# Performance work log

Hardware: AMD Instinct MI355X
Metric: run time of the kernel (lower is better)

Reference implementation:

```python
import jax, jax.numpy as jnp
import numpy as np

B, L, D = 1, 2048, 1024
H = 16
HD = D // H
BETA = 0.08
EPS = 1e-6


def setup_inputs() -> dict:
    key = jax.random.key(0)
    ks = jax.random.split(key, 12)
    sc = 1.0 / np.sqrt(D)
    inp = {
        'x': jax.random.normal(ks[0], (B, L, D), dtype=jnp.float32),
        'Wq': jax.random.normal(ks[1], (D, D), dtype=jnp.float32) * sc,
        'bq': jnp.zeros((D,), jnp.float32),
        'Wk': jax.random.normal(ks[2], (D, D), dtype=jnp.float32) * sc,
        'bk': jnp.zeros((D,), jnp.float32),
        'Wv': jax.random.normal(ks[3], (D, D), dtype=jnp.float32) * sc,
        'bv': jnp.zeros((D,), jnp.float32),
        'Wo': jax.random.normal(ks[4], (D, D), dtype=jnp.float32) * sc,
        'bo': jnp.zeros((D,), jnp.float32),
        'Wp': jax.random.normal(ks[5], (2 * H, D), dtype=jnp.float32) * sc,
        'bp': jnp.zeros((2 * H,), jnp.float32),
        'gamma': jnp.full((H,), -2.197224577, jnp.float32),
    }
    return inp


def _split(t):  # [B,L,D] -> [B,H,L,hd]
    return t.reshape(B, L, H, HD).transpose(0, 2, 1, 3)


def reference(x, Wq, bq, Wk, bk, Wv, bv, Wo, bo, Wp, bp, gamma):
    q = _split(x @ Wq.T + bq)
    k = _split(x @ Wk.T + bk)
    v = _split(x @ Wv.T + bv)

    # phase features: [B,L,2H] -> [B,H,L,2], L2-normalized (torch F.normalize: x / max(||x||, eps))
    ph = (x @ Wp.T + bp).reshape(B, L, H, 2).transpose(0, 2, 1, 3)
    nrm = jnp.maximum(jnp.linalg.norm(ph, axis=-1, keepdims=True), EPS)
    ph = ph / nrm
    c, s = ph[..., 0], ph[..., 1]  # [B,H,L]

    # rank-2 Gram interference bias: cos(dphi) = c_i c_j + s_i s_j -> [B,H,L,L]
    inter = c[..., :, None] * c[..., None, :] + s[..., :, None] * s[..., None, :]
    head_gate = jax.nn.sigmoid(gamma) * BETA  # active_heads_mask all ones (fraction=1.0)
    bias = inter * head_gate[None, :, None, None]

    scores = jnp.einsum('bhqd,bhkd->bhqk', q, k) / jnp.sqrt(jnp.float32(HD)) + bias
    attn = jax.nn.softmax(scores, axis=-1)
    out = jnp.einsum('bhqk,bhkd->bhqd', attn, v)
    out = out.transpose(0, 2, 1, 3).reshape(B, L, D)
    return out @ Wo.T + bo
```

## Files before the change

### kernel.cpp

```cpp
#include <hip/hip_runtime.h>
#include <stdint.h>

typedef unsigned short u16;
typedef unsigned int u32;

#define L_SEQ 2048
#define DMODEL 1024
#define NHEAD 16

using f32x4 = __attribute__((ext_vector_type(4))) float;
using f32x16 = __attribute__((ext_vector_type(16))) float;
using s16x8 = __attribute__((ext_vector_type(8))) short;
using s16x4 = __attribute__((ext_vector_type(4))) short;

__device__ __forceinline__ u16 f2b(float f) {
    union { float f; uint32_t u; } v; v.f = f;
    uint32_t r = v.u + 0x7fffu + ((v.u >> 16) & 1u);
    return (u16)(r >> 16);
}

__device__ __forceinline__ float b2f(u16 x) {
    union { uint32_t u; float f; } v; v.u = ((uint32_t)x) << 16;
    return v.f;
}

__device__ __forceinline__ u32 pk2(float a, float b) {
    return (u32)f2b(a) | ((u32)f2b(b) << 16);
}

__device__ __forceinline__ u32 cvtpk(float lo, float hi_) {
    u32 r;
    asm("v_cvt_pk_bf16_f32 %0, %1, %2" : "=v"(r) : "v"(lo), "v"(hi_));
    return r;
}

__device__ __forceinline__ void gld16(const void* g, void* l) {
    __builtin_amdgcn_global_load_lds(
        (__attribute__((address_space(1))) void*)(uintptr_t)g,
        (__attribute__((address_space(3))) void*)(uintptr_t)l,
        16, 0, 0);
}

__global__ __launch_bounds__(256)
void k_pre(const float* __restrict__ x, const float* __restrict__ wq,
           const float* __restrict__ wk, const float* __restrict__ wv,
           const float* __restrict__ wo,
           u16* __restrict__ xb, u16* __restrict__ wqb, u16* __restrict__ wkb,
           u16* __restrict__ wvb, u16* __restrict__ wob,
           const float* __restrict__ Wp, const float* __restrict__ bp,
           float2* __restrict__ CSph) {
    const int NX = L_SEQ * DMODEL / 8;
    const int NW = DMODEL * DMODEL / 8;
    const int NCONV = (NX + 4 * NW) / 256;
    const int tid = threadIdx.x;
    __shared__ float pbuf[4][32];

    if ((int)blockIdx.x < NCONV) {
        int i = blockIdx.x * 256 + tid;
        const float* src; u16* dst; int j;
        if (i < NX) { src = x; dst = xb; j = i; }
        else {
            int t = i - NX; int sel = t >> 17; j = t & (NW - 1);
            src = (sel == 0) ? wq : (sel == 1) ? wk : (sel == 2) ? wv : wo;
            dst = (sel == 0) ? wqb : (sel == 1) ? wkb : (sel == 2) ? wvb : wob;
        }
        const float4* s4 = (const float4*)src;
        float4 a = s4[2 * j], b = s4[2 * j + 1];
        union { s16x8 v; u16 u[8]; } o;
        o.u[0] = f2b(a.x); o.u[1] = f2b(a.y); o.u[2] = f2b(a.z); o.u[3] = f2b(a.w);
        o.u[4] = f2b(b.x); o.u[5] = f2b(b.y); o.u[6] = f2b(b.z); o.u[7] = f2b(b.w);
        ((s16x8*)dst)[j] = o.v;
        return;
    }

    const int w = tid >> 6, lane = tid & 63;
    const int m = (blockIdx.x - NCONV) * 4 + w;
    float xr[16];
#pragma unroll
    for (int i = 0; i < 16; ++i) xr[i] = x[(size_t)m * DMODEL + lane + 64 * i];
#pragma unroll 4
    for (int n = 0; n < 32; ++n) {
        const float* wrow = Wp + n * DMODEL;
        float s = 0.f;
#pragma unroll
        for (int i = 0; i < 16; ++i) s += xr[i] * wrow[lane + 64 * i];
#pragma unroll
        for (int msk = 32; msk >= 1; msk >>= 1) s += __shfl_xor(s, msk);
        if (lane == 0) pbuf[w][n] = s + bp[n];
    }
    __syncthreads();
    if (lane < 16) {
        float c = pbuf[w][2 * lane], sn = pbuf[w][2 * lane + 1];
        float nrm = sqrtf(c * c + sn * sn);
        float inv = 1.0f / fmaxf(nrm, 1e-6f);
        CSph[(size_t)lane * L_SEQ + m] = make_float2(c * inv, sn * inv);
    }
}

template <int MODE>
__global__ __launch_bounds__(256, 2)
void k_gemm64(const u16* __restrict__ A,
              const u16* __restrict__ B0, const u16* __restrict__ B1, const u16* __restrict__ B2,
              const float* __restrict__ c0, const float* __restrict__ c1, const float* __restrict__ c2,
              void* __restrict__ Out, u16* __restrict__ Vt, int ldo, int K) {
    __shared__ u16 As[128 * 64];
    __shared__ u16 Bs[64 * 64];
    const int tid = threadIdx.x;
    const int w = tid >> 6, lane = tid & 63;
    const int wr = w >> 1, wc = w & 1;
    const int u = lane & 15, g = lane >> 4;
    const int lr = lane >> 3;
    const int cb = lane & 7;
    const int mt = blockIdx.x, nt = blockIdx.y;
    const int seg = nt >> 4, ntl = nt & 15;
    const u16* Bp = (seg == 0) ? B0 : (seg == 1) ? B1 : B2;
    const float* biasp = (seg == 0) ? c0 : (seg == 1) ? c1 : c2;

    const u16* Ab = A + (size_t)(mt * 128 + w * 32) * K;
    const u16* Bb = Bp + (size_t)(ntl * 64) * K;
    char* asB = (char*)As;
    char* bsB = (char*)Bs;

    f32x4 acc[4][2] = {};

    for (int k0 = 0; k0 < K; k0 += 64) {
#pragma unroll
        for (int c = 0; c < 4; ++c)
            gld16(Ab + (size_t)(c * 8 + lr) * K + k0 + ((cb ^ lr) * 8),
                  asB + (w * 32 + c * 8) * 128);
#pragma unroll
        for (int t = 0; t < 2; ++t)
            gld16(Bb + (size_t)(t * 32 + w * 8 + lr) * K + k0 + ((cb ^ lr) * 8),
                  bsB + t * 4096 + w * 1024);
        __syncthreads();
        const int x0 = (g * 16) ^ ((u & 7) << 4);
#pragma unroll
        for (int ks = 0; ks < 2; ++ks) {
            s16x8 af[4], bf[2];
#pragma unroll
            for (int i = 0; i < 4; ++i)
                af[i] = *(const s16x8*)(asB + (wr * 64 + i * 16 + u) * 128 + (x0 ^ (ks * 64)));
#pragma unroll
            for (int j = 0; j < 2; ++j)
                bf[j] = *(const s16x8*)(bsB + (wc * 32 + j * 16 + u) * 128 + (x0 ^ (ks * 64)));
#pragma unroll
            for (int i = 0; i < 4; ++i)
#pragma unroll
                for (int j = 0; j < 2; ++j)
                    acc[i][j] = __builtin_amdgcn_mfma_f32_16x16x32_bf16(af[i], bf[j], acc[i][j], 0, 0, 0);
        }
        __syncthreads();
    }

#pragma unroll
    for (int i = 0; i < 4; ++i) {
#pragma unroll
        for (int j = 0; j < 2; ++j) {
            const int row0 = mt * 128 + wr * 64 + i * 16 + g * 4;
            const int col = nt * 64 + wc * 32 + j * 16 + u;
            const int colseg = ntl * 64 + wc * 32 + j * 16 + u;
            const float bias = biasp[colseg];
            if (MODE == 0 && seg == 2) {
                union { s16x4 v; u16 us[4]; } p;
#pragma unroll
                for (int r = 0; r < 4; ++r) p.us[r] = f2b(acc[i][j][r] + bias);
                *(s16x4*)(Vt + (size_t)colseg * L_SEQ + row0) = p.v;
            } else {
#pragma unroll
                for (int r = 0; r < 4; ++r) {
                    float val = acc[i][j][r] + bias;
                    if (MODE == 1)
                        ((float*)Out)[(size_t)(row0 + r) * ldo + col] = val;
                    else
                        ((u16*)Out)[(size_t)(row0 + r) * ldo + col] = f2b(val);
                }
            }
        }
    }
}

__global__ __launch_bounds__(256, 2)
void k_attn(const u16* __restrict__ QKV, const u16* __restrict__ VtG,
            const float2* __restrict__ CSph,
            const float* __restrict__ gamma,
            u16* __restrict__ Op0, u16* __restrict__ Op1, u16* __restrict__ Op2,
            float2* __restrict__ ML) {
    const int h = blockIdx.y;
    const int s = blockIdx.z;
    const int qb = blockIdx.x * 128;
    const int tid = threadIdx.x;
    const int ww = tid >> 6, lane = tid & 63;
    const int q5 = lane & 31, hi = lane >> 5;
    const int ld = 3 * DMODEL;
    const int NT = (s == 2) ? 10 : 11;
    const int kbase = s * 11 * 64;
    const int BUF = 64 * 64 * 2;

    __shared__ u16 Ks[2][64 * 64];
    __shared__ u16 Vs[2][64 * 64];

    const float LOG2E = 1.44269504088896f;
    const float sig = 1.0f / (1.0f + __expf(-gamma[h]));
    const float gateA = 0.64f * sig;
    const float SC2 = 0.125f * LOG2E;

    const u16* Qp = QKV + h * 64;
    const u16* Kp = QKV + DMODEL + h * 64 + (size_t)kbase * ld;
    const u16* VtH = VtG + (size_t)h * 64 * L_SEQ + kbase;
    const float2* CS = CSph + (size_t)h * L_SEQ;

    const int qrow = qb + ww * 32 + q5;
    s16x8 bq[4];
#pragma unroll
    for (int d = 0; d < 4; ++d)
        bq[d] = *(const s16x8*)(Qp + (size_t)qrow * ld + d * 16 + hi * 8);
    s16x8 bcs;
    {
        float2 cs = CS[qrow];
        union { u32 w[4]; s16x8 v; } t = {};
        t.w[0] = hi ? 0u : pk2(cs.x, cs.y);
        bcs = t.v;
    }

    unsigned dstOff[2]; size_t srcK[2], srcV[2];
#pragma unroll
    for (int t = 0; t < 2; ++t) {
        int ci = (ww * 2 + t) * 64 + lane;
        int row = ci >> 3, cb = ci & 7;
        dstOff[t] = (unsigned)((ww * 2 + t) * 1024);
        srcK[t] = (size_t)row * ld + (size_t)((cb ^ (row & 7)) * 8);
        srcV[t] = (size_t)row * L_SEQ + (size_t)((cb ^ (row & 7)) * 8);
    }
    char* ksBase = (char*)Ks;
    char* vsBase = (char*)Vs;
    const int swz = (q5 & 7) << 4;

#pragma unroll
    for (int t = 0; t < 2; ++t) {
        gld16(Kp + srcK[t], ksBase + dstOff[t]);
        gld16(VtH + srcV[t], vsBase + dstOff[t]);
    }
    __syncthreads();

    float m = -1e30f;
    float lsum = 0.f;
    f32x16 oA = {}, oB = {};

    for (int kt = 0; kt < NT; ++kt) {
        const int cur = kt & 1;
        const char* kCur = ksBase + cur * BUF;
        const char* vCur = vsBase + cur * BUF;

        if (kt + 1 < NT) {
            const u16* Kn = Kp + (size_t)(kt + 1) * 64 * ld;
            const u16* Vn = VtH + (size_t)(kt + 1) * 64;
            char* kN = ksBase + (cur ^ 1) * BUF;
            char* vN = vsBase + (cur ^ 1) * BUF;
#pragma unroll
            for (int t = 0; t < 2; ++t) {
                gld16(Kn + srcK[t], kN + dstOff[t]);
                gld16(Vn + srcV[t], vN + dstOff[t]);
            }
        }

        s16x8 acs0, acs1;
        {
            float2 c0 = CS[kbase + kt * 64 + q5];
            float2 c1 = CS[kbase + kt * 64 + 32 + q5];
            union { u32 w[4]; s16x8 v; } t0 = {}, t1 = {};
            t0.w[0] = hi ? 0u : pk2(gateA * c0.x, gateA * c0.y);
            t1.w[0] = hi ? 0u : pk2(gateA * c1.x, gateA * c1.y);
            acs0 = t0.v; acs1 = t1.v;
        }

        f32x16 sf0 = {}, sf1 = {};
        __builtin_amdgcn_s_setprio(1);
#pragma unroll
        for (int d = 0; d < 4; ++d) {
            s16x8 ak0 = *(const s16x8*)(kCur + q5 * 128 + ((d * 32 + hi * 16) ^ swz));
            s16x8 ak1 = *(const s16x8*)(kCur + (32 + q5) * 128 + ((d * 32 + hi * 16) ^ swz));
            sf0 = __builtin_amdgcn_mfma_f32_32x32x16_bf16(ak0, bq[d], sf0, 0, 0, 0);
            sf1 = __builtin_amdgcn_mfma_f32_32x32x16_bf16(ak1, bq[d], sf1, 0, 0, 0);
        }
        sf0 = __builtin_amdgcn_mfma_f32_32x32x16_bf16(acs0, bcs, sf0, 0, 0, 0);
        sf1 = __builtin_amdgcn_mfma_f32_32x32x16_bf16(acs1, bcs, sf1, 0, 0, 0);
        __builtin_amdgcn_s_setprio(0);

        float tl = fmaxf(sf0[0], sf1[0]);
#pragma unroll
        for (int r = 1; r < 16; ++r) tl = fmaxf(tl, fmaxf(sf0[r], sf1[r]));
        tl = fmaxf(tl, __shfl_xor(tl, 32));
        float tlx = tl * SC2;

        if (__any(tlx > m + 4.0f)) {
            float mn = fmaxf(m, tlx);
            float scl = __builtin_amdgcn_exp2f(m - mn);
            m = mn;
            float sclr[16];
#pragma unroll
            for (int r = 0; r < 16; ++r)
                sclr[r] = __shfl(scl, (r & 3) + 8 * (r >> 2) + 4 * hi);
#pragma unroll
            for (int r = 0; r < 16; ++r) { oA[r] *= sclr[r]; oB[r] *= sclr[r]; }
            lsum *= scl;
        }

#pragma unroll
        for (int r = 0; r < 16; ++r) sf0[r] = __builtin_amdgcn_exp2f(__builtin_fmaf(sf0[r], SC2, -m));
#pragma unroll
        for (int r = 0; r < 16; ++r) sf1[r] = __builtin_amdgcn_exp2f(__builtin_fmaf(sf1[r], SC2, -m));

        float lps = 0.f;
#pragma unroll
        for (int r = 0; r < 16; ++r) lps += sf0[r] + sf1[r];
        lsum += lps + __shfl_xor(lps, 32);

        __builtin_amdgcn_s_setprio(1);
#define PV_SUBTILE(SFV, HALF, SU)                                                              \
        {                                                                                      \
            u32 Aw  = cvtpk(SFV[(HALF) * 8 + 0], SFV[(HALF) * 8 + 1]);                         \
            u32 A2w = cvtpk(SFV[(HALF) * 8 + 2], SFV[(HALF) * 8 + 3]);                         \
            u32 Bw  = cvtpk(SFV[(HALF) * 8 + 4], SFV[(HALF) * 8 + 5]);                         \
            u32 B2w = cvtpk(SFV[(HALF) * 8 + 6], SFV[(HALF) * 8 + 7]);                         \
            u32 xw  = (u32)__shfl_xor((int)(hi ? Aw : Bw), 32);                                \
            u32 x2w = (u32)__shfl_xor((int)(hi ? A2w : B2w), 32);                              \
            union { u32 w[4]; s16x8 v; } pa;                                                   \
            pa.w[0] = hi ? xw : Aw;   pa.w[1] = hi ? x2w : A2w;                                \
            pa.w[2] = hi ? Bw : xw;   pa.w[3] = hi ? B2w : x2w;                                \
            s16x8 bvA = *(const s16x8*)(vCur + q5 * 128 + (((SU) * 32 + hi * 16) ^ swz));      \
            s16x8 bvB = *(const s16x8*)(vCur + (32 + q5) * 128 + (((SU) * 32 + hi * 16) ^ swz));\
            oA = __builtin_amdgcn_mfma_f32_32x32x16_bf16(pa.v, bvA, oA, 0, 0, 0);              \
            oB = __builtin_amdgcn_mfma_f32_32x32x16_bf16(pa.v, bvB, oB, 0, 0, 0);              \
        }
        PV_SUBTILE(sf0, 0, 0)
        PV_SUBTILE(sf0, 1, 1)
        PV_SUBTILE(sf1, 0, 2)
        PV_SUBTILE(sf1, 1, 3)
#undef PV_SUBTILE
        __builtin_amdgcn_s_setprio(0);

        __syncthreads();
    }

    u16* OpS = (s == 0) ? Op0 : (s == 1) ? Op1 : Op2;
    float2* MLS = ML + (size_t)(s * NHEAD + h) * L_SEQ;
#pragma unroll
    for (int r = 0; r < 16; ++r) {
        int q_r = qb + ww * 32 + (r & 3) + 8 * (r >> 2) + 4 * hi;
        OpS[(size_t)q_r * DMODEL + h * 64 + q5] = f2b(oA[r]);
        OpS[(size_t)q_r * DMODEL + h * 64 + 32 + q5] = f2b(oB[r]);
    }
    if (hi == 0)
        MLS[qb + ww * 32 + q5] = make_float2(m, lsum);
}

__global__ __launch_bounds__(256)
void k_comb(const u16* __restrict__ Op0, const u16* __restrict__ Op1,
            const u16* __restrict__ Op2, const float2* __restrict__ ML,
            u16* __restrict__ attnb) {
    int t = blockIdx.x * 256 + threadIdx.x;
    int row = t >> 7, cg = t & 127;
    int col0 = cg * 8, h = cg >> 3;
    float2 ml0 = ML[(size_t)h * L_SEQ + row];
    float2 ml1 = ML[(size_t)(NHEAD + h) * L_SEQ + row];
    float2 ml2 = ML[(size_t)(2 * NHEAD + h) * L_SEQ + row];
    float M = fmaxf(fmaxf(ml0.x, ml1.x), ml2.x);
    float a0 = __builtin_amdgcn_exp2f(ml0.x - M);
    float a1 = __builtin_amdgcn_exp2f(ml1.x - M);
    float a2 = __builtin_amdgcn_exp2f(ml2.x - M);
    float inv = 1.0f / (ml0.y * a0 + ml1.y * a1 + ml2.y * a2);
    a0 *= inv; a1 *= inv; a2 *= inv;
    union { s16x8 v; u16 us[8]; } o0, o1, o2, wout;
    size_t off = (size_t)row * DMODEL + col0;
    o0.v = *(const s16x8*)(Op0 + off);
    o1.v = *(const s16x8*)(Op1 + off);
    o2.v = *(const s16x8*)(Op2 + off);
#pragma unroll
    for (int j = 0; j < 8; ++j)
        wout.us[j] = f2b(b2f(o0.us[j]) * a0 + b2f(o1.us[j]) * a1 + b2f(o2.us[j]) * a2);
    *(s16x8*)(attnb + off) = wout.v;
}

extern "C" void kernel_launch(void* const* d_in, const int* in_sizes, int n_in,
                              void* d_out, int out_size, void* d_ws, size_t ws_size,
                              hipStream_t stream) {
    const float* x  = (const float*)d_in[0];
    const float* Wq = (const float*)d_in[1];
    const float* bq = (const float*)d_in[2];
    const float* Wk = (const float*)d_in[3];
    const float* bk = (const float*)d_in[4];
    const float* Wv = (const float*)d_in[5];
    const float* bv = (const float*)d_in[6];
    const float* Wo = (const float*)d_in[7];
    const float* bo = (const float*)d_in[8];
    const float* Wp = (const float*)d_in[9];
    const float* bp = (const float*)d_in[10];
    const float* gamma = (const float*)d_in[11];
    float* out = (float*)d_out;

    char* ws = (char*)d_ws;
    u16* xb = (u16*)ws;   ws += (size_t)L_SEQ * DMODEL * 2;
    u16* wqb = (u16*)ws;  ws += (size_t)DMODEL * DMODEL * 2;
    u16* wkb = (u16*)ws;  ws += (size_t)DMODEL * DMODEL * 2;
    u16* wvb = (u16*)ws;  ws += (size_t)DMODEL * DMODEL * 2;
    u16* wob = (u16*)ws;  ws += (size_t)DMODEL * DMODEL * 2;
    u16* qkv = (u16*)ws;  ws += (size_t)L_SEQ * 3 * DMODEL * 2;
    u16* attnb = (u16*)ws; ws += (size_t)L_SEQ * DMODEL * 2;
    u16* VtG = (u16*)ws;  ws += (size_t)DMODEL * L_SEQ * 2;
    float2* CSph = (float2*)ws; ws += (size_t)NHEAD * L_SEQ * 8;

    u16* Op0 = xb;
    u16* Op1 = wqb;
    u16* Op2 = attnb;
    float2* ML = (float2*)wvb;

    k_pre<<<3072 + 512, 256, 0, stream>>>(x, Wq, Wk, Wv, Wo, xb, wqb, wkb, wvb, wob,
                                          Wp, bp, CSph);

    k_gemm64<0><<<dim3(16, 48), 256, 0, stream>>>(xb, wqb, wkb, wvb, bq, bk, bv,
                                                  (void*)qkv, VtG, 3 * DMODEL, DMODEL);

    k_attn<<<dim3(L_SEQ / 128, NHEAD, 3), 256, 0, stream>>>(qkv, VtG, CSph, gamma,
                                                            Op0, Op1, Op2, ML);

    k_comb<<<L_SEQ * DMODEL / 8 / 256, 256, 0, stream>>>(Op0, Op1, Op2, ML, attnb);

    k_gemm64<1><<<dim3(16, 16), 256, 0, stream>>>(attnb, wob, wob, wob, bo, bo, bo,
                                                  (void*)out, nullptr, DMODEL, DMODEL);
}
```

Measured before the change: 106.1 us.

## Fold phase projection into QKV bf16 GEMM and add separate normalize kernel

The scalar fp32 phase projection (x @ Wp.T) previously computed in k_pre with per-wave shuffle reductions is moved into the QKV MFMA GEMM as a fourth 64-column segment. Wp is converted to bf16 and zero-padded to 64 rows. A new small kernel then L2-normalizes the pair outputs into CSph. This removes the slow wave-per-row dot-product blocks from the preprocessing kernel. In exchange it adds a kernel launch and a scratch buffer, and lowers the phase projection to bf16 precision.

```diff
diff --git a/kernel.cpp b/kernel.cpp
--- a/kernel.cpp
+++ b/kernel.cpp
@@ -42,21 +42,21 @@
 }
 
 __global__ __launch_bounds__(256)
-void k_pre(const float* __restrict__ x, const float* __restrict__ wq,
-           const float* __restrict__ wk, const float* __restrict__ wv,
-           const float* __restrict__ wo,
-           u16* __restrict__ xb, u16* __restrict__ wqb, u16* __restrict__ wkb,
-           u16* __restrict__ wvb, u16* __restrict__ wob,
-           const float* __restrict__ Wp, const float* __restrict__ bp,
-           float2* __restrict__ CSph) {
+void k_conv(const float* __restrict__ x, const float* __restrict__ wq,
+            const float* __restrict__ wk, const float* __restrict__ wv,
+            const float* __restrict__ wo, const float* __restrict__ wp,
+            const float* __restrict__ bp,
+            u16* __restrict__ xb, u16* __restrict__ wqb, u16* __restrict__ wkb,
+            u16* __restrict__ wvb, u16* __restrict__ wob, u16* __restrict__ wpb,
+            float* __restrict__ bpPad) {
     const int NX = L_SEQ * DMODEL / 8;
     const int NW = DMODEL * DMODEL / 8;
     const int NCONV = (NX + 4 * NW) / 256;
-    const int tid = threadIdx.x;
-    __shared__ float pbuf[4][32];
-
-    if ((int)blockIdx.x < NCONV) {
-        int i = blockIdx.x * 256 + tid;
+    const int NP = 32 * DMODEL / 8;
+    const int bid = blockIdx.x, tid = threadIdx.x;
+
+    if (bid < NCONV) {
+        int i = bid * 256 + tid;
         const float* src; u16* dst; int j;
         if (i < NX) { src = x; dst = xb; j = i; }
         else {
@@ -72,37 +72,33 @@
         ((s16x8*)dst)[j] = o.v;
         return;
     }
-
-    const int w = tid >> 6, lane = tid & 63;
-    const int m = (blockIdx.x - NCONV) * 4 + w;
-    float xr[16];
-#pragma unroll
-    for (int i = 0; i < 16; ++i) xr[i] = x[(size_t)m * DMODEL + lane + 64 * i];
-#pragma unroll 4
-    for (int n = 0; n < 32; ++n) {
-        const float* wrow = Wp + n * DMODEL;
-        float s = 0.f;
-#pragma unroll
-        for (int i = 0; i < 16; ++i) s += xr[i] * wrow[lane + 64 * i];
-#pragma unroll
-        for (int msk = 32; msk >= 1; msk >>= 1) s += __shfl_xor(s, msk);
-        if (lane == 0) pbuf[w][n] = s + bp[n];
-    }
-    __syncthreads();
-    if (lane < 16) {
-        float c = pbuf[w][2 * lane], sn = pbuf[w][2 * lane + 1];
-        float nrm = sqrtf(c * c + sn * sn);
-        float inv = 1.0f / fmaxf(nrm, 1e-6f);
-        CSph[(size_t)lane * L_SEQ + m] = make_float2(c * inv, sn * inv);
-    }
+    if (bid < NCONV + 32) {
+        int i2 = (bid - NCONV) * 256 + tid;
+        union { s16x8 v; u16 u[8]; } o;
+        if (i2 < NP) {
+            const float4* s4 = (const float4*)wp;
+            float4 a = s4[2 * i2], b = s4[2 * i2 + 1];
+            o.u[0] = f2b(a.x); o.u[1] = f2b(a.y); o.u[2] = f2b(a.z); o.u[3] = f2b(a.w);
+            o.u[4] = f2b(b.x); o.u[5] = f2b(b.y); o.u[6] = f2b(b.z); o.u[7] = f2b(b.w);
+        } else {
+#pragma unroll
+            for (int j = 0; j < 8; ++j) o.u[j] = 0;
+        }
+        ((s16x8*)wpb)[i2] = o.v;
+        return;
+    }
+    if (tid < 64) bpPad[tid] = (tid < 32) ? bp[tid] : 0.f;
 }
 
 template <int MODE>
 __global__ __launch_bounds__(256, 2)
 void k_gemm64(const u16* __restrict__ A,
               const u16* __restrict__ B0, const u16* __restrict__ B1, const u16* __restrict__ B2,
+              const u16* __restrict__ B3,
               const float* __restrict__ c0, const float* __restrict__ c1, const float* __restrict__ c2,
-              void* __restrict__ Out, u16* __restrict__ Vt, int ldo, int K) {
+              const float* __restrict__ c3,
+              void* __restrict__ Out, u16* __restrict__ Vt, float* __restrict__ Ph,
+              int ldo, int K) {
     __shared__ u16 As[128 * 64];
     __shared__ u16 Bs[64 * 64];
     const int tid = threadIdx.x;
@@ -113,8 +109,8 @@
     const int cb = lane & 7;
     const int mt = blockIdx.x, nt = blockIdx.y;
     const int seg = nt >> 4, ntl = nt & 15;
-    const u16* Bp = (seg == 0) ? B0 : (seg == 1) ? B1 : B2;
-    const float* biasp = (seg == 0) ? c0 : (seg == 1) ? c1 : c2;
+    const u16* Bp = (seg == 0) ? B0 : (seg == 1) ? B1 : (seg == 2) ? B2 : B3;
+    const float* biasp = (seg == 0) ? c0 : (seg == 1) ? c1 : (seg == 2) ? c2 : c3;
 
     const u16* Ab = A + (size_t)(mt * 128 + w * 32) * K;
     const u16* Bb = Bp + (size_t)(ntl * 64) * K;
@@ -165,6 +161,10 @@
 #pragma unroll
                 for (int r = 0; r < 4; ++r) p.us[r] = f2b(acc[i][j][r] + bias);
                 *(s16x4*)(Vt + (size_t)colseg * L_SEQ + row0) = p.v;
+            } else if (MODE == 0 && seg == 3) {
+#pragma unroll
+                for (int r = 0; r < 4; ++r)
+                    Ph[(size_t)(row0 + r) * 64 + colseg] = acc[i][j][r] + bias;
             } else {
 #pragma unroll
                 for (int r = 0; r < 4; ++r) {
@@ -177,6 +177,16 @@
             }
         }
     }
+}
+
+__global__ __launch_bounds__(256)
+void k_norm(const float* __restrict__ ph, float2* __restrict__ CSph) {
+    int t = blockIdx.x * 256 + threadIdx.x;
+    int m = t >> 4, h = t & 15;
+    float c = ph[(size_t)m * 64 + 2 * h];
+    float s = ph[(size_t)m * 64 + 2 * h + 1];
+    float inv = 1.0f / fmaxf(sqrtf(c * c + s * s), 1e-6f);
+    CSph[(size_t)h * L_SEQ + m] = make_float2(c * inv, s * inv);
 }
 
 __global__ __launch_bounds__(256, 2)
@@ -408,23 +418,30 @@
     u16* attnb = (u16*)ws; ws += (size_t)L_SEQ * DMODEL * 2;
     u16* VtG = (u16*)ws;  ws += (size_t)DMODEL * L_SEQ * 2;
     float2* CSph = (float2*)ws; ws += (size_t)NHEAD * L_SEQ * 8;
+    u16* wpb = (u16*)ws;  ws += (size_t)64 * DMODEL * 2;
+    float* bpPad = (float*)ws; ws += 64 * 4;
+    float* phtmp = (float*)ws; ws += (size_t)L_SEQ * 64 * 4;
 
     u16* Op0 = xb;
     u16* Op1 = wqb;
     u16* Op2 = attnb;
     float2* ML = (float2*)wvb;
 
-    k_pre<<<3072 + 512, 256, 0, stream>>>(x, Wq, Wk, Wv, Wo, xb, wqb, wkb, wvb, wob,
-                                          Wp, bp, CSph);
-
-    k_gemm64<0><<<dim3(16, 48), 256, 0, stream>>>(xb, wqb, wkb, wvb, bq, bk, bv,
-                                                  (void*)qkv, VtG, 3 * DMODEL, DMODEL);
+    k_conv<<<3072 + 32 + 1, 256, 0, stream>>>(x, Wq, Wk, Wv, Wo, Wp, bp,
+                                              xb, wqb, wkb, wvb, wob, wpb, bpPad);
+
+    k_gemm64<0><<<dim3(16, 49), 256, 0, stream>>>(xb, wqb, wkb, wvb, wpb,
+                                                  bq, bk, bv, bpPad,
+                                                  (void*)qkv, VtG, phtmp, 3 * DMODEL, DMODEL);
+
+    k_norm<<<L_SEQ * NHEAD / 256, 256, 0, stream>>>(phtmp, CSph);
 
     k_attn<<<dim3(L_SEQ / 128, NHEAD, 3), 256, 0, stream>>>(qkv, VtG, CSph, gamma,
                                                             Op0, Op1, Op2, ML);
 
     k_comb<<<L_SEQ * DMODEL / 8 / 256, 256, 0, stream>>>(Op0, Op1, Op2, ML, attnb);
 
-    k_gemm64<1><<<dim3(16, 16), 256, 0, stream>>>(attnb, wob, wob, wob, bo, bo, bo,
-                                                  (void*)out, nullptr, DMODEL, DMODEL);
-}
+    k_gemm64<1><<<dim3(16, 16), 256, 0, stream>>>(attnb, wob, wob, wob, wob,
+                                                  bo, bo, bo, bo,
+                                                  (void*)out, nullptr, nullptr, DMODEL, DMODEL);
+}
```

After: 88.70 us. 1.2x faster.
